# Kernel optimization log

Measured on AMD Instinct MI355X. Metric: run time of the kernel, lower is better.

## Reference

```python
import jax, jax.numpy as jnp
import numpy as np

N, D = 16384, 32            # nodes, max neighbors (0-padded)
INP, U = 256, 128           # input_units, units
R, ENT = 8, 8               # relations, entity types (relation/entity id 0 = padding for relations)


def setup_inputs() -> dict:
    key = jax.random.key(0)
    ks = jax.random.split(key, 12)
    s = 0.05  # scale learned params for numerical sanity (torch init is raw randn)
    return {
        "node_state": jax.random.normal(ks[0], (N, INP), dtype=jnp.float32),
        "adjacency": jax.random.randint(ks[1], (N, D), 0, N + 1, dtype=jnp.int32),  # 0 = pad row
        "point_enc": jax.random.randint(ks[2], (N,), 0, ENT, dtype=jnp.int32),
        "relation_enc": jax.random.randint(ks[3], (N, D), 0, R, dtype=jnp.int32),   # 0 = pad edge
        "point_enc_w": jax.random.normal(ks[4], (ENT, INP, U), dtype=jnp.float32) * s,
        "relation_enc_w": jax.random.normal(ks[5], (R, U, U), dtype=jnp.float32) * s,
        "q_w": jax.random.normal(ks[6], (U, U), dtype=jnp.float32) * s,
        "k_w": jax.random.normal(ks[7], (U, U), dtype=jnp.float32) * s,
        "v_w": jax.random.normal(ks[8], (U, U), dtype=jnp.float32) * s,
        "fc_w": jax.random.normal(ks[9], (U, U), dtype=jnp.float32) * s,
        "fc_b": jax.random.normal(ks[10], (U,), dtype=jnp.float32) * s,
    }


def reference(node_state, adjacency, point_enc, relation_enc,
              point_enc_w, relation_enc_w, q_w, k_w, v_w, fc_w, fc_b):
    ent, inp, u = point_enc_w.shape
    r_cnt = relation_enc_w.shape[0]
    dt = node_state.dtype

    # center = node_state @ point_enc_w[point_enc]; loop over small fixed entity set
    # to avoid materializing an (N, INP, U) gathered weight tensor.
    center = jnp.zeros((node_state.shape[0], u), dtype=dt)
    for e in range(ent):
        center = center + jnp.where(point_enc[:, None] == e,
                                    node_state @ point_enc_w[e], 0.0)

    # prepend zero row: adjacency index 0 == padding neighbor
    padded = jnp.concatenate([jnp.zeros((1, u), dtype=dt), center], axis=0)  # (N+1, U)
    x = padded[adjacency]  # (N, D, U) gathered neighbor embeddings

    # neighbors = x @ relation_enc_w[relation_enc]; per-relation GEMM + mask
    # (same math as the per-edge gathered matmul, without the E*U*U blowup)
    neighbors = jnp.zeros_like(x)
    for r in range(r_cnt):
        neighbors = neighbors + jnp.where(relation_enc[..., None] == r,
                                          jnp.einsum('ndu,uv->ndv', x, relation_enc_w[r]), 0.0)

    scale = u ** 0.5
    q = (center @ q_w) / scale                               # (N, U)
    k = jnp.einsum('ndu,uv->ndv', neighbors, k_w) / scale    # (N, D, U)
    v = jnp.einsum('ndu,uv->ndv', neighbors, v_w)            # (N, D, U)

    scores = jnp.einsum('nu,ndu->nd', q, k)                  # (N, D)
    scores = jnp.where(relation_enc == 0, jnp.asarray(-1e9, dt), scores)
    attn = jax.nn.softmax(scores, axis=-1)                   # over neighbors
    agg = jnp.einsum('nd,ndu->nu', attn, v)                  # (N, U)

    return center + jax.nn.relu(agg @ fc_w + fc_b)           # (N, U)
```

## Files before the change

kernel.cpp:

```cpp
#include <hip/hip_runtime.h>

#define NNODE 16384
#define DD 32
#define INPC 256
#define UC 128
#define RC 8
#define EC 8

typedef __attribute__((ext_vector_type(8))) short short8;
typedef __attribute__((ext_vector_type(4))) float float4v;

__device__ __forceinline__ unsigned short f2bf(float f) {
    unsigned u = __builtin_bit_cast(unsigned, f);
    unsigned r = (u + 0x7FFFu + ((u >> 16) & 1u)) >> 16;
    return (unsigned short)r;
}
__device__ __forceinline__ float bflo(unsigned u) { return __builtin_bit_cast(float, u << 16); }
__device__ __forceinline__ float bfhi(unsigned u) { return __builtin_bit_cast(float, u & 0xFFFF0000u); }
__device__ __forceinline__ float bf2f(unsigned short s) { return __builtin_bit_cast(float, (unsigned)s << 16); }

__device__ __forceinline__ int bfrag_idx(int k, int col, int nct) {
    int ks = k >> 5, ct = col >> 4;
    int l = (((k >> 3) & 3) << 4) | (col & 15);
    return (((ks * nct + ct) << 6) + l) * 8 + (k & 7);
}

__global__ void k_setup(const float* __restrict__ pew, const float* __restrict__ qw,
                        const float* __restrict__ kw, const float* __restrict__ relw,
                        const float* __restrict__ vw, const float* __restrict__ fcw,
                        const int* __restrict__ pe,
                        unsigned short* __restrict__ pewfrag,
                        unsigned short* __restrict__ BallQfrag, unsigned short* __restrict__ RVFfrag,
                        int* __restrict__ blockhist) {
    __shared__ float P_s[16 * 128];
    __shared__ int hh[8];
    int b = blockIdx.x;
    if (b < 1024) {
        int id = b * 256 + threadIdx.x;
        int e = id >> 15, k = (id >> 7) & 255, col = id & 127;
        pewfrag[(e << 15) + bfrag_idx(k, col, 8)] = f2bf(pew[id]);
        return;
    }
    if (b < 1088) {
        int pb = b - 1024;
        int r = pb & 7, i0 = (pb >> 3) * 16;
        int j = threadIdx.x & 127, h = threadIdx.x >> 7;
        {
            float acc[8] = {0,0,0,0,0,0,0,0};
            const float4* kr = (const float4*)(kw + j * UC);
            for (int lc = 0; lc < 32; ++lc) {
                float4 bb = kr[lc];
                #pragma unroll
                for (int ii = 0; ii < 8; ++ii) {
                    float4 a = *(const float4*)&qw[(i0 + h * 8 + ii) * UC + lc * 4];
                    acc[ii] += a.x * bb.x + a.y * bb.y + a.z * bb.z + a.w * bb.w;
                }
            }
            #pragma unroll
            for (int ii = 0; ii < 8; ++ii)
                P_s[(h * 8 + ii) * 128 + j] = acc[ii] * (1.0f / 128.0f);
        }
        __syncthreads();

        const float* R = relw + r * UC * UC;
        float accM[8] = {0,0,0,0,0,0,0,0};
        for (int mc = 0; mc < 32; ++mc) {
            float4 rv = *(const float4*)&R[j * UC + mc * 4];
            #pragma unroll
            for (int ii = 0; ii < 8; ++ii) {
                float4 p = *(const float4*)&P_s[(h * 8 + ii) * 128 + mc * 4];
                accM[ii] += p.x * rv.x + p.y * rv.y + p.z * rv.z + p.w * rv.w;
            }
        }
        #pragma unroll
        for (int ii = 0; ii < 8; ++ii)
            BallQfrag[bfrag_idx(i0 + h * 8 + ii, r * 128 + j, 64)] = f2bf(accM[ii]);

        float accV[8] = {0,0,0,0,0,0,0,0};
        for (int m = 0; m < UC; ++m) {
            float v = vw[m * UC + j];
            #pragma unroll
            for (int ii = 0; ii < 8; ++ii)
                accV[ii] += R[(i0 + h * 8 + ii) * UC + m] * v;
        }
        __syncthreads();
        #pragma unroll
        for (int ii = 0; ii < 8; ++ii)
            P_s[(h * 8 + ii) * 128 + j] = accV[ii];
        __syncthreads();

        float accF[8] = {0,0,0,0,0,0,0,0};
        for (int m = 0; m < UC; ++m) {
            float w = fcw[m * UC + j];
            #pragma unroll
            for (int ii = 0; ii < 8; ++ii)
                accF[ii] += P_s[(h * 8 + ii) * 128 + m] * w;
        }
        #pragma unroll
        for (int ii = 0; ii < 8; ++ii)
            RVFfrag[bfrag_idx(r * 128 + i0 + h * 8 + ii, j, 8)] = f2bf(accF[ii]);
        return;
    }
    {
        int hb = b - 1088;
        if (threadIdx.x < 8) hh[threadIdx.x] = 0;
        __syncthreads();
        atomicAdd(&hh[pe[hb * 256 + threadIdx.x]], 1);
        __syncthreads();
        if (threadIdx.x < 8) blockhist[hb * 8 + threadIdx.x] = hh[threadIdx.x];
    }
}

__global__ void k_scatter(const int* __restrict__ pe, const int* __restrict__ blockhist,
                          int* __restrict__ list, int* __restrict__ cnt, int* __restrict__ basep) {
    __shared__ int boff[8];
    __shared__ int totS[8], exS[8];
    __shared__ int wavecnt[4 * 8];
    int t = threadIdx.x, w = t >> 6, l = t & 63;
    if (w == 0) {
        #pragma unroll
        for (int e = 0; e < 8; ++e) {
            int h = blockhist[l * 8 + e];
            int pref = h;
            #pragma unroll
            for (int off = 1; off < 64; off <<= 1) {
                int v = __shfl_up(pref, off, 64);
                pref += (l >= off) ? v : 0;
            }
            if (l == (int)blockIdx.x) exS[e] = pref - h;
            if (l == 63) totS[e] = pref;
        }
    }
    __syncthreads();
    if (t == 0) {
        int run = 0;
        #pragma unroll
        for (int e = 0; e < 8; ++e) {
            boff[e] = run + exS[e];
            if (blockIdx.x == 0) { basep[e] = run; cnt[e] = totS[e]; }
            run += totS[e];
        }
    }
    __syncthreads();
    int n = blockIdx.x * 256 + t;
    int e = pe[n];
    unsigned long long mymask = 0;
    #pragma unroll
    for (int r = 0; r < 8; ++r) {
        unsigned long long m = __ballot(e == r);
        if (e == r) mymask = m;
        if (l == r) wavecnt[w * 8 + r] = (int)__popcll(m);
    }
    __syncthreads();
    int off = 0;
    for (int w2 = 0; w2 < w; ++w2) off += wavecnt[w2 * 8 + e];
    unsigned long long ltmask = (1ull << l) - 1ull;
    int rank = (int)__popcll(mymask & ltmask);
    list[boff[e] + off + rank] = n;
}

__global__ __launch_bounds__(256, 4)
void k_center(const float* __restrict__ ns, const unsigned short* __restrict__ pewfrag,
              const int* __restrict__ list, const int* __restrict__ cnt,
              const int* __restrict__ base, unsigned short* __restrict__ center_bf) {
    int e = blockIdx.y;
    int c = cnt[e];
    int start = blockIdx.x * 16;
    if (start >= c) return;
    int w = threadIdx.x >> 6, l = threadIdx.x & 63;

    int rid = list[base[e] + min(start + (l & 15), c - 1)];

    float4v acc[2] = {};
    const unsigned short* pf = pewfrag + ((size_t)e << 15);
    #pragma unroll
    for (int ks = 0; ks < 8; ++ks) {
        const float* ap = &ns[(size_t)rid * 256 + ks * 32 + ((l >> 4) << 3)];
        float4 v0 = *(const float4*)ap;
        float4 v1 = *(const float4*)(ap + 4);
        short8 a;
        a[0] = f2bf(v0.x); a[1] = f2bf(v0.y); a[2] = f2bf(v0.z); a[3] = f2bf(v0.w);
        a[4] = f2bf(v1.x); a[5] = f2bf(v1.y); a[6] = f2bf(v1.z); a[7] = f2bf(v1.w);
        #pragma unroll
        for (int ci = 0; ci < 2; ++ci) {
            int ct = w * 2 + ci;
            short8 b = *(const short8*)&pf[(((ks * 8 + ct) << 6) + l) * 8];
            acc[ci] = __builtin_amdgcn_mfma_f32_16x16x32_bf16(a, b, acc[ci], 0, 0, 0);
        }
    }
    #pragma unroll
    for (int reg = 0; reg < 4; ++reg) {
        int row16 = start + ((l >> 4) << 2) + reg;
        if (row16 < c) {
            int gid = list[base[e] + row16];
            #pragma unroll
            for (int ci = 0; ci < 2; ++ci)
                center_bf[(size_t)gid * 128 + (w * 2 + ci) * 16 + (l & 15)] = f2bf(acc[ci][reg]);
        }
    }
}

#define QSTRIDE 1096
__global__ __launch_bounds__(256, 4)
void k_final(const unsigned short* __restrict__ center_bf,
             const unsigned short* __restrict__ BallQfrag,
             const unsigned short* __restrict__ RVFfrag,
             const int* __restrict__ adj, const int* __restrict__ rel,
             const float* __restrict__ fcb, float* __restrict__ out) {
    __shared__ unsigned short qlds[16 * QSTRIDE];
    __shared__ unsigned edata[4][32][2];
    int w = threadIdx.x >> 6, l = threadIdx.x & 63;
    int n0 = blockIdx.x * 16;

    {
        short8 a[4];
        #pragma unroll
        for (int ks = 0; ks < 4; ++ks)
            a[ks] = *(const short8*)&center_bf[(size_t)(n0 + (l & 15)) * 128 + ks * 32 + ((l >> 4) << 3)];
        for (int ci = 0; ci < 16; ++ci) {
            int ct = w * 16 + ci;
            float4v acc = {};
            #pragma unroll
            for (int ks = 0; ks < 4; ++ks) {
                short8 b = *(const short8*)&BallQfrag[(((ks * 64 + ct) << 6) + l) * 8];
                acc = __builtin_amdgcn_mfma_f32_16x16x32_bf16(a[ks], b, acc, 0, 0, 0);
            }
            int r = ct >> 3;
            int ch = (ct & 7) * 16 + (l & 15);
            #pragma unroll
            for (int reg = 0; reg < 4; ++reg) {
                int rn = ((l >> 4) << 2) + reg;
                qlds[rn * QSTRIDE + r * 136 + ch] = f2bf(acc[reg]);
            }
        }
    }
    __syncthreads();

    for (int q = 0; q < 4; ++q) {
        int tn = w * 4 + q;
        int n = n0 + tn;
        int ai[2], rv[2], rowv[2];
        #pragma unroll
        for (int t = 0; t < 2; ++t) {
            ai[t] = adj[n * DD + t * 16 + (l & 15)];
            rv[t] = rel[n * DD + t * 16 + (l & 15)];
            rowv[t] = ai[t] > 0 ? ai[t] - 1 : 0;
        }
        float4v sc[2] = {};
        #pragma unroll
        for (int ks = 0; ks < 4; ++ks) {
            short8 qb = *(const short8*)&qlds[tn * QSTRIDE + (l & 7) * 136 + ks * 32 + ((l >> 4) << 3)];
            #pragma unroll
            for (int t = 0; t < 2; ++t) {
                short8 xa = *(const short8*)&center_bf[(size_t)rowv[t] * 128 + ks * 32 + ((l >> 4) << 3)];
                sc[t] = __builtin_amdgcn_mfma_f32_16x16x32_bf16(xa, qb, sc[t], 0, 0, 0);
            }
        }
        float sel[2][4];
        int ai2[2][4];
        #pragma unroll
        for (int t = 0; t < 2; ++t)
            #pragma unroll
            for (int reg = 0; reg < 4; ++reg) {
                int e2l = ((l >> 4) & 3) * 4 + reg;
                int rd2 = __shfl(rv[t], (l & 48) | e2l, 64);
                ai2[t][reg] = __shfl(ai[t], (l & 48) | e2l, 64);
                float s = __shfl(sc[t][reg], (l & 48) | rd2, 64);
                if (ai2[t][reg] == 0) s = 0.f;
                if (rd2 == 0) s = -1e9f;
                sel[t][reg] = s;
            }
        float mx = sel[0][0];
        #pragma unroll
        for (int t = 0; t < 2; ++t)
            #pragma unroll
            for (int reg = 0; reg < 4; ++reg) mx = fmaxf(mx, sel[t][reg]);
        mx = fmaxf(mx, __shfl_xor(mx, 16, 64));
        mx = fmaxf(mx, __shfl_xor(mx, 32, 64));
        float at[2][4];
        float sm = 0.f;
        #pragma unroll
        for (int t = 0; t < 2; ++t)
            #pragma unroll
            for (int reg = 0; reg < 4; ++reg) {
                at[t][reg] = __expf(sel[t][reg] - mx);
                sm += at[t][reg];
            }
        sm += __shfl_xor(sm, 16, 64);
        sm += __shfl_xor(sm, 32, 64);
        float inv = 1.0f / sm;
        #pragma unroll
        for (int t = 0; t < 2; ++t)
            #pragma unroll
            for (int reg = 0; reg < 4; ++reg) {
                at[t][reg] *= inv;
                if (ai2[t][reg] == 0) at[t][reg] = 0.f;
            }

        #pragma unroll
        for (int rg = 0; rg < 4; ++rg) {
            if (l == (l >> 4) * 20 + rg) {
                #pragma unroll
                for (int t = 0; t < 2; ++t) {
                    uint2 md;
                    md.x = __builtin_bit_cast(unsigned, at[t][rg]);
                    md.y = ((unsigned)rowv[t] << 3) | (unsigned)rv[t];
                    *(uint2*)&edata[w][t * 16 + (l & 15)][0] = md;
                }
            }
        }

        float bk0[8], bk1[8];
        #pragma unroll
        for (int r = 0; r < 8; ++r) { bk0[r] = 0.f; bk1[r] = 0.f; }
        #pragma unroll
        for (int d = 0; d < 32; ++d) {
            uint2 md = *(const uint2*)&edata[w][d][0];
            float ad = __builtin_bit_cast(float, md.x);
            int rowe = (int)(md.y >> 3);
            int rve = (int)(md.y & 7u);
            unsigned xu = *(const unsigned*)&center_bf[(size_t)rowe * 128 + l * 2];
            float x0 = bflo(xu), x1 = bfhi(xu);
            #pragma unroll
            for (int r = 0; r < 8; ++r) {
                float am = (rve == r) ? ad : 0.f;
                bk0[r] += am * x0;
                bk1[r] += am * x1;
            }
        }
        #pragma unroll
        for (int r = 0; r < 8; ++r) {
            unsigned pk = (unsigned)f2bf(bk0[r]) | ((unsigned)f2bf(bk1[r]) << 16);
            *(unsigned*)&qlds[tn * QSTRIDE + r * 128 + l * 2] = pk;
        }
    }
    __syncthreads();

    #pragma unroll
    for (int ci = 0; ci < 2; ++ci) {
        int ct = w * 2 + ci;
        float4v acc = {};
        #pragma unroll 4
        for (int ks = 0; ks < 32; ++ks) {
            short8 a = *(const short8*)&qlds[(l & 15) * QSTRIDE + ks * 32 + ((l >> 4) << 3)];
            short8 b = *(const short8*)&RVFfrag[(((ks * 8 + ct) << 6) + l) * 8];
            acc = __builtin_amdgcn_mfma_f32_16x16x32_bf16(a, b, acc, 0, 0, 0);
        }
        int col = ct * 16 + (l & 15);
        float bb = fcb[col];
        #pragma unroll
        for (int reg = 0; reg < 4; ++reg) {
            int n = n0 + ((l >> 4) << 2) + reg;
            float v = acc[reg] + bb;
            v = v > 0.f ? v : 0.f;
            out[(size_t)n * 128 + col] = bf2f(center_bf[(size_t)n * 128 + col]) + v;
        }
    }
}

extern "C" void kernel_launch(void* const* d_in, const int* in_sizes, int n_in,
                              void* d_out, int out_size, void* d_ws, size_t ws_size,
                              hipStream_t stream) {
    const float* node_state = (const float*)d_in[0];
    const int*   adjacency  = (const int*)d_in[1];
    const int*   point_enc  = (const int*)d_in[2];
    const int*   relation   = (const int*)d_in[3];
    const float* pew        = (const float*)d_in[4];
    const float* relw       = (const float*)d_in[5];
    const float* qw         = (const float*)d_in[6];
    const float* kw         = (const float*)d_in[7];
    const float* vw         = (const float*)d_in[8];
    const float* fcw        = (const float*)d_in[9];
    const float* fcb        = (const float*)d_in[10];
    float* out = (float*)d_out;

    char* ws = (char*)d_ws;
    unsigned short* BallQfrag = (unsigned short*)ws;  ws += 128 * 1024 * 2;
    unsigned short* RVFfrag   = (unsigned short*)ws;  ws += 1024 * 128 * 2;
    unsigned short* center_bf = (unsigned short*)ws;  ws += (size_t)NNODE * 128 * 2;
    unsigned short* pewfrag   = (unsigned short*)ws;  ws += 8 * 32768 * 2;
    int* blockhist            = (int*)ws;             ws += 64 * 8 * 4;
    int* cnt                  = (int*)ws;             ws += 32;
    int* basep                = (int*)ws;             ws += 32;
    int* list                 = (int*)ws;             ws += NNODE * 4;

    k_setup<<<1152, 256, 0, stream>>>(pew, qw, kw, relw, vw, fcw, point_enc,
                                      pewfrag, BallQfrag, RVFfrag, blockhist);
    k_scatter<<<64, 256, 0, stream>>>(point_enc, blockhist, list, cnt, basep);
    k_center<<<dim3(192, 8), 256, 0, stream>>>(node_state, pewfrag, list, cnt, basep, center_bf);
    k_final<<<NNODE / 16, 256, 0, stream>>>(center_bf, BallQfrag, RVFfrag,
                                            adjacency, relation, fcb, out);
}
```

Measured before the change: 197.2 us.

## Use MFMA for weight-fusion setup GEMMs and per-relation neighbor aggregation

```diff
diff --git a/kernel.cpp b/kernel.cpp
--- a/kernel.cpp
+++ b/kernel.cpp
@@ -9,15 +9,25 @@
 
 typedef __attribute__((ext_vector_type(8))) short short8;
 typedef __attribute__((ext_vector_type(4))) float float4v;
+typedef __attribute__((ext_vector_type(4))) unsigned uint4v;
 
 __device__ __forceinline__ unsigned short f2bf(float f) {
     unsigned u = __builtin_bit_cast(unsigned, f);
     unsigned r = (u + 0x7FFFu + ((u >> 16) & 1u)) >> 16;
     return (unsigned short)r;
 }
-__device__ __forceinline__ float bflo(unsigned u) { return __builtin_bit_cast(float, u << 16); }
-__device__ __forceinline__ float bfhi(unsigned u) { return __builtin_bit_cast(float, u & 0xFFFF0000u); }
 __device__ __forceinline__ float bf2f(unsigned short s) { return __builtin_bit_cast(float, (unsigned)s << 16); }
+
+__device__ __forceinline__ short8 ld8bf(const float* p) {
+    float4 v0 = *(const float4*)p;
+    float4 v1 = *(const float4*)(p + 4);
+    short8 a;
+    a[0] = (short)f2bf(v0.x); a[1] = (short)f2bf(v0.y);
+    a[2] = (short)f2bf(v0.z); a[3] = (short)f2bf(v0.w);
+    a[4] = (short)f2bf(v1.x); a[5] = (short)f2bf(v1.y);
+    a[6] = (short)f2bf(v1.z); a[7] = (short)f2bf(v1.w);
+    return a;
+}
 
 __device__ __forceinline__ int bfrag_idx(int k, int col, int nct) {
     int ks = k >> 5, ct = col >> 4;
@@ -32,7 +42,8 @@
                         unsigned short* __restrict__ pewfrag,
                         unsigned short* __restrict__ BallQfrag, unsigned short* __restrict__ RVFfrag,
                         int* __restrict__ blockhist) {
-    __shared__ float P_s[16 * 128];
+    __shared__ unsigned short stage_s[128 * 132];
+    __shared__ unsigned short mat_s[16 * 136];
     __shared__ int hh[8];
     int b = blockIdx.x;
     if (b < 1024) {
@@ -44,61 +55,112 @@
     if (b < 1088) {
         int pb = b - 1024;
         int r = pb & 7, i0 = (pb >> 3) * 16;
-        int j = threadIdx.x & 127, h = threadIdx.x >> 7;
-        {
-            float acc[8] = {0,0,0,0,0,0,0,0};
-            const float4* kr = (const float4*)(kw + j * UC);
-            for (int lc = 0; lc < 32; ++lc) {
-                float4 bb = kr[lc];
+        int w = threadIdx.x >> 6, l = threadIdx.x & 63;
+        int mrow = l & 15, kgrp = (l >> 4) << 3;
+        const float* R = relw + r * (UC * UC);
+
+        float4v accP[2] = {};
+        #pragma unroll
+        for (int ks = 0; ks < 4; ++ks) {
+            short8 a = ld8bf(&qw[(i0 + mrow) * UC + ks * 32 + kgrp]);
+            #pragma unroll
+            for (int ci = 0; ci < 2; ++ci) {
+                int ct = w * 2 + ci;
+                short8 bf = ld8bf(&kw[(ct * 16 + mrow) * UC + ks * 32 + kgrp]);
+                accP[ci] = __builtin_amdgcn_mfma_f32_16x16x32_bf16(a, bf, accP[ci], 0, 0, 0);
+            }
+        }
+        #pragma unroll
+        for (int ci = 0; ci < 2; ++ci)
+            #pragma unroll
+            for (int reg = 0; reg < 4; ++reg) {
+                int row = ((l >> 4) << 2) + reg;
+                int col = (w * 2 + ci) * 16 + mrow;
+                mat_s[row * 136 + col] = f2bf(accP[ci][reg] * (1.0f / 128.0f));
+            }
+        for (int it = 0; it < 16; ++it) {
+            int idx = it * 256 + threadIdx.x;
+            int row = idx >> 5, col = (idx & 31) * 4;
+            float4 v = *(const float4*)&vw[row * UC + col];
+            uint2 o;
+            o.x = (unsigned)f2bf(v.x) | ((unsigned)f2bf(v.y) << 16);
+            o.y = (unsigned)f2bf(v.z) | ((unsigned)f2bf(v.w) << 16);
+            *(uint2*)&stage_s[row * 132 + col] = o;
+        }
+        __syncthreads();
+
+        float4v accM[2] = {}, accV[2] = {};
+        #pragma unroll
+        for (int ks = 0; ks < 4; ++ks) {
+            short8 aM = *(const short8*)&mat_s[mrow * 136 + ks * 32 + kgrp];
+            short8 aV = ld8bf(&R[(i0 + mrow) * UC + ks * 32 + kgrp]);
+            #pragma unroll
+            for (int ci = 0; ci < 2; ++ci) {
+                int ct = w * 2 + ci;
+                short8 bM = ld8bf(&R[(ct * 16 + mrow) * UC + ks * 32 + kgrp]);
+                accM[ci] = __builtin_amdgcn_mfma_f32_16x16x32_bf16(aM, bM, accM[ci], 0, 0, 0);
+                uint4v pv;
                 #pragma unroll
-                for (int ii = 0; ii < 8; ++ii) {
-                    float4 a = *(const float4*)&qw[(i0 + h * 8 + ii) * UC + lc * 4];
-                    acc[ii] += a.x * bb.x + a.y * bb.y + a.z * bb.z + a.w * bb.w;
+                for (int jp = 0; jp < 4; ++jp) {
+                    unsigned e0 = stage_s[(ks * 32 + kgrp + jp * 2) * 132 + ct * 16 + mrow];
+                    unsigned e1 = stage_s[(ks * 32 + kgrp + jp * 2 + 1) * 132 + ct * 16 + mrow];
+                    pv[jp] = e0 | (e1 << 16);
                 }
-            }
-            #pragma unroll
-            for (int ii = 0; ii < 8; ++ii)
-                P_s[(h * 8 + ii) * 128 + j] = acc[ii] * (1.0f / 128.0f);
-        }
+                accV[ci] = __builtin_amdgcn_mfma_f32_16x16x32_bf16(
+                    aV, __builtin_bit_cast(short8, pv), accV[ci], 0, 0, 0);
+            }
+        }
+        #pragma unroll
+        for (int ci = 0; ci < 2; ++ci)
+            #pragma unroll
+            for (int reg = 0; reg < 4; ++reg) {
+                int i = i0 + ((l >> 4) << 2) + reg;
+                int col = r * 128 + (w * 2 + ci) * 16 + mrow;
+                BallQfrag[bfrag_idx(i, col, 64)] = f2bf(accM[ci][reg]);
+            }
         __syncthreads();
-
-        const float* R = relw + r * UC * UC;
-        float accM[8] = {0,0,0,0,0,0,0,0};
-        for (int mc = 0; mc < 32; ++mc) {
-            float4 rv = *(const float4*)&R[j * UC + mc * 4];
-            #pragma unroll
-            for (int ii = 0; ii < 8; ++ii) {
-                float4 p = *(const float4*)&P_s[(h * 8 + ii) * 128 + mc * 4];
-                accM[ii] += p.x * rv.x + p.y * rv.y + p.z * rv.z + p.w * rv.w;
-            }
-        }
-        #pragma unroll
-        for (int ii = 0; ii < 8; ++ii)
-            BallQfrag[bfrag_idx(i0 + h * 8 + ii, r * 128 + j, 64)] = f2bf(accM[ii]);
-
-        float accV[8] = {0,0,0,0,0,0,0,0};
-        for (int m = 0; m < UC; ++m) {
-            float v = vw[m * UC + j];
-            #pragma unroll
-            for (int ii = 0; ii < 8; ++ii)
-                accV[ii] += R[(i0 + h * 8 + ii) * UC + m] * v;
+        #pragma unroll
+        for (int ci = 0; ci < 2; ++ci)
+            #pragma unroll
+            for (int reg = 0; reg < 4; ++reg)
+                mat_s[(((l >> 4) << 2) + reg) * 136 + (w * 2 + ci) * 16 + mrow] = f2bf(accV[ci][reg]);
+        for (int it = 0; it < 16; ++it) {
+            int idx = it * 256 + threadIdx.x;
+            int row = idx >> 5, col = (idx & 31) * 4;
+            float4 v = *(const float4*)&fcw[row * UC + col];
+            uint2 o;
+            o.x = (unsigned)f2bf(v.x) | ((unsigned)f2bf(v.y) << 16);
+            o.y = (unsigned)f2bf(v.z) | ((unsigned)f2bf(v.w) << 16);
+            *(uint2*)&stage_s[row * 132 + col] = o;
         }
         __syncthreads();
-        #pragma unroll
-        for (int ii = 0; ii < 8; ++ii)
-            P_s[(h * 8 + ii) * 128 + j] = accV[ii];
-        __syncthreads();
-
-        float accF[8] = {0,0,0,0,0,0,0,0};
-        for (int m = 0; m < UC; ++m) {
-            float w = fcw[m * UC + j];
-            #pragma unroll
-            for (int ii = 0; ii < 8; ++ii)
-                accF[ii] += P_s[(h * 8 + ii) * 128 + m] * w;
-        }
-        #pragma unroll
-        for (int ii = 0; ii < 8; ++ii)
-            RVFfrag[bfrag_idx(r * 128 + i0 + h * 8 + ii, j, 8)] = f2bf(accF[ii]);
+
+        float4v accF[2] = {};
+        #pragma unroll
+        for (int ks = 0; ks < 4; ++ks) {
+            short8 aF = *(const short8*)&mat_s[mrow * 136 + ks * 32 + kgrp];
+            #pragma unroll
+            for (int ci = 0; ci < 2; ++ci) {
+                int ct = w * 2 + ci;
+                uint4v pv;
+                #pragma unroll
+                for (int jp = 0; jp < 4; ++jp) {
+                    unsigned e0 = stage_s[(ks * 32 + kgrp + jp * 2) * 132 + ct * 16 + mrow];
+                    unsigned e1 = stage_s[(ks * 32 + kgrp + jp * 2 + 1) * 132 + ct * 16 + mrow];
+                    pv[jp] = e0 | (e1 << 16);
+                }
+                accF[ci] = __builtin_amdgcn_mfma_f32_16x16x32_bf16(
+                    aF, __builtin_bit_cast(short8, pv), accF[ci], 0, 0, 0);
+            }
+        }
+        #pragma unroll
+        for (int ci = 0; ci < 2; ++ci)
+            #pragma unroll
+            for (int reg = 0; reg < 4; ++reg) {
+                int i = i0 + ((l >> 4) << 2) + reg;
+                int col = (w * 2 + ci) * 16 + mrow;
+                RVFfrag[bfrag_idx(r * 128 + i, col, 8)] = f2bf(accF[ci][reg]);
+            }
         return;
     }
     {
@@ -175,12 +237,7 @@
     const unsigned short* pf = pewfrag + ((size_t)e << 15);
     #pragma unroll
     for (int ks = 0; ks < 8; ++ks) {
-        const float* ap = &ns[(size_t)rid * 256 + ks * 32 + ((l >> 4) << 3)];
-        float4 v0 = *(const float4*)ap;
-        float4 v1 = *(const float4*)(ap + 4);
-        short8 a;
-        a[0] = f2bf(v0.x); a[1] = f2bf(v0.y); a[2] = f2bf(v0.z); a[3] = f2bf(v0.w);
-        a[4] = f2bf(v1.x); a[5] = f2bf(v1.y); a[6] = f2bf(v1.z); a[7] = f2bf(v1.w);
+        short8 a = ld8bf(&ns[(size_t)rid * 256 + ks * 32 + ((l >> 4) << 3)]);
         #pragma unroll
         for (int ci = 0; ci < 2; ++ci) {
             int ct = w * 2 + ci;
@@ -208,7 +265,7 @@
              const int* __restrict__ adj, const int* __restrict__ rel,
              const float* __restrict__ fcb, float* __restrict__ out) {
     __shared__ unsigned short qlds[16 * QSTRIDE];
-    __shared__ unsigned edata[4][32][2];
+    __shared__ uint2 edata[4][32];
     int w = threadIdx.x >> 6, l = threadIdx.x & 63;
     int n0 = blockIdx.x * 16;
 
@@ -303,35 +360,49 @@
                 #pragma unroll
                 for (int t = 0; t < 2; ++t) {
                     uint2 md;
-                    md.x = __builtin_bit_cast(unsigned, at[t][rg]);
-                    md.y = ((unsigned)rowv[t] << 3) | (unsigned)rv[t];
-                    *(uint2*)&edata[w][t * 16 + (l & 15)][0] = md;
+                    md.x = (unsigned)rowv[t];
+                    md.y = (unsigned)f2bf(at[t][rg]) | ((unsigned)rv[t] << 16);
+                    edata[w][t * 16 + (l & 15)] = md;
                 }
             }
         }
 
-        float bk0[8], bk1[8];
-        #pragma unroll
-        for (int r = 0; r < 8; ++r) { bk0[r] = 0.f; bk1[r] = 0.f; }
-        #pragma unroll
-        for (int d = 0; d < 32; ++d) {
-            uint2 md = *(const uint2*)&edata[w][d][0];
-            float ad = __builtin_bit_cast(float, md.x);
-            int rowe = (int)(md.y >> 3);
-            int rve = (int)(md.y & 7u);
-            unsigned xu = *(const unsigned*)&center_bf[(size_t)rowe * 128 + l * 2];
-            float x0 = bflo(xu), x1 = bfhi(xu);
-            #pragma unroll
-            for (int r = 0; r < 8; ++r) {
-                float am = (rve == r) ? ad : 0.f;
-                bk0[r] += am * x0;
-                bk1[r] += am * x1;
-            }
-        }
-        #pragma unroll
-        for (int r = 0; r < 8; ++r) {
-            unsigned pk = (unsigned)f2bf(bk0[r]) | ((unsigned)f2bf(bk1[r]) << 16);
-            *(unsigned*)&qlds[tn * QSTRIDE + r * 128 + l * 2] = pk;
+        unsigned aw[4];
+        int rows[8];
+        #pragma unroll
+        for (int jp = 0; jp < 4; ++jp) {
+            uint2 m0 = edata[w][((l >> 4) << 3) + jp * 2];
+            uint2 m1 = edata[w][((l >> 4) << 3) + jp * 2 + 1];
+            unsigned s0 = ((m0.y >> 16) == (unsigned)(l & 15)) ? (m0.y & 0xFFFFu) : 0u;
+            unsigned s1 = ((m1.y >> 16) == (unsigned)(l & 15)) ? (m1.y & 0xFFFFu) : 0u;
+            aw[jp] = s0 | (s1 << 16);
+            rows[jp * 2] = (int)m0.x;
+            rows[jp * 2 + 1] = (int)m1.x;
+        }
+        uint4v av = {aw[0], aw[1], aw[2], aw[3]};
+        short8 afrag = __builtin_bit_cast(short8, av);
+        const unsigned short* xb0 = center_bf + (size_t)rows[0] * 128 + (l & 15);
+        const unsigned short* xb1 = center_bf + (size_t)rows[1] * 128 + (l & 15);
+        const unsigned short* xb2 = center_bf + (size_t)rows[2] * 128 + (l & 15);
+        const unsigned short* xb3 = center_bf + (size_t)rows[3] * 128 + (l & 15);
+        const unsigned short* xb4 = center_bf + (size_t)rows[4] * 128 + (l & 15);
+        const unsigned short* xb5 = center_bf + (size_t)rows[5] * 128 + (l & 15);
+        const unsigned short* xb6 = center_bf + (size_t)rows[6] * 128 + (l & 15);
+        const unsigned short* xb7 = center_bf + (size_t)rows[7] * 128 + (l & 15);
+        #pragma unroll
+        for (int ct = 0; ct < 8; ++ct) {
+            unsigned p0 = xb0[ct * 16], p1 = xb1[ct * 16], p2 = xb2[ct * 16], p3 = xb3[ct * 16];
+            unsigned p4 = xb4[ct * 16], p5 = xb5[ct * 16], p6 = xb6[ct * 16], p7 = xb7[ct * 16];
+            uint4v bv = {p0 | (p1 << 16), p2 | (p3 << 16), p4 | (p5 << 16), p6 | (p7 << 16)};
+            float4v zc = {};
+            float4v acc = __builtin_amdgcn_mfma_f32_16x16x32_bf16(
+                afrag, __builtin_bit_cast(short8, bv), zc, 0, 0, 0);
+            if (l < 32) {
+                int rbase = (l >> 4) << 2;
+                #pragma unroll
+                for (int reg = 0; reg < 4; ++reg)
+                    qlds[tn * QSTRIDE + (rbase + reg) * 136 + ct * 16 + (l & 15)] = f2bf(acc[reg]);
+            }
         }
     }
     __syncthreads();
@@ -342,7 +413,8 @@
         float4v acc = {};
         #pragma unroll 4
         for (int ks = 0; ks < 32; ++ks) {
-            short8 a = *(const short8*)&qlds[(l & 15) * QSTRIDE + ks * 32 + ((l >> 4) << 3)];
+            short8 a = *(const short8*)&qlds[(l & 15) * QSTRIDE + (ks >> 2) * 136
+                                             + (ks & 3) * 32 + ((l >> 4) << 3)];
             short8 b = *(const short8*)&RVFfrag[(((ks * 8 + ct) << 6) + l) * 8];
             acc = __builtin_amdgcn_mfma_f32_16x16x32_bf16(a, b, acc, 0, 0, 0);
         }
```

Result: faster. 164.9 us (-16.4%).
